# Optimization experiments

Measured on AMD Instinct MI355X. Metric: run time of the kernel, lower is better.

Reference implementation:

```python
import jax, jax.numpy as jnp
import numpy as np

B, S, H, D = 2, 2048, 16, 128
HID = H * D
ROPE_BASE = 10000.0


def _rope_tables(seq_len, dim, dtype):
    inv_freq = 1.0 / (ROPE_BASE ** (jnp.arange(0, dim, 2, dtype=jnp.float32) / dim))
    t = jnp.arange(seq_len, dtype=jnp.float32)
    freqs = jnp.einsum('s,d->sd', t, inv_freq)          # [S, D/2]
    emb = jnp.concatenate([freqs, freqs], axis=-1)       # [S, D]
    return jnp.cos(emb).astype(dtype), jnp.sin(emb).astype(dtype)


def _rotate_half(x):
    x1, x2 = jnp.split(x, 2, axis=-1)
    return jnp.concatenate([-x2, x1], axis=-1)


def _apply_rope(x, cos, sin, position_ids):
    # x: [B,H,S,D]; cos/sin: [S_emb, D]; position_ids: [B,S] or [1,S]
    c = cos[position_ids][:, None, :, :]  # [B,1,S,D]
    s = sin[position_ids][:, None, :, :]
    return x * c + _rotate_half(x) * s


def setup_inputs() -> dict:
    key = jax.random.key(0)
    ks = jax.random.split(key, 9)
    hidden_states = jax.random.normal(ks[0], (B, S, HID), jnp.float32) * 0.02
    Wq = jax.random.normal(ks[1], (HID, HID), jnp.float32) * 0.02
    Wk = jax.random.normal(ks[2], (HID, HID), jnp.float32) * 0.02
    Wv = jax.random.normal(ks[3], (HID, HID), jnp.float32) * 0.02
    Wo = jax.random.normal(ks[4], (HID, HID), jnp.float32) * 0.02
    # binary mask marking summary tokens
    sum_mask = jax.random.randint(ks[5], (B, S), 0, 2).astype(jnp.float32)
    # row-stochastic-ish averaging matrix over tokens (KV compression weights)
    raw = jax.random.uniform(ks[6], (B, S, S), jnp.float32)
    sum_attn_mask = sum_mask[:, :, None] * raw / jnp.sum(raw, axis=-1, keepdims=True)
    # additive causal mask [B,1,S,S]
    causal = jnp.tril(jnp.ones((S, S), dtype=bool))
    attention_mask = jnp.where(causal, 0.0, -1e9).astype(jnp.float32)
    attention_mask = jnp.broadcast_to(attention_mask[None, None], (B, 1, S, S))
    position_ids = jnp.broadcast_to(jnp.arange(S, dtype=jnp.int32), (B, S))
    return {
        'hidden_states': hidden_states, 'sum_mask': sum_mask,
        'sum_attn_mask': sum_attn_mask, 'attention_mask': attention_mask,
        'position_ids': position_ids, 'Wq': Wq, 'Wk': Wk, 'Wv': Wv, 'Wo': Wo,
    }


def reference(hidden_states, sum_mask, sum_attn_mask, attention_mask,
              position_ids, Wq, Wk, Wv, Wo):
    dtype = hidden_states.dtype
    # projections (F.linear: x @ W^T), then [B,H,S,D]
    def proj(W):
        return (hidden_states @ W.T).reshape(B, S, H, D).transpose(0, 2, 1, 3)
    q, k, v = proj(Wq), proj(Wk), proj(Wv)

    kv_seq_len = S
    cos, sin = _rope_tables(kv_seq_len, D, dtype)
    q = _apply_rope(q, cos, sin, position_ids)

    # KV compression: weighted token averaging injected at summary positions
    k_avg = jnp.einsum('bqk,bhkd->bhqd', sum_attn_mask, k)
    v_avg = jnp.einsum('bqk,bhkd->bhqd', sum_attn_mask, v)
    no_sum = (1.0 - sum_mask)[:, None, :, None]  # [B,1,S,1]
    k = no_sum * k + k_avg
    v = no_sum * v + v_avg

    key_pos = jnp.arange(kv_seq_len, dtype=jnp.int32)[None, :]  # [1,S]
    k = _apply_rope(k, cos, sin, key_pos)

    scale = 1.0 / np.sqrt(D)
    attn = jnp.einsum('bhqd,bhkd->bhqk', q, k) * scale
    attn = attn + attention_mask
    attn = jnp.maximum(attn, jnp.finfo(attn.dtype).min)
    attn = jax.nn.softmax(attn.astype(jnp.float32), axis=-1).astype(dtype)
    out = jnp.einsum('bhqk,bhkd->bhqd', attn, v)            # [B,H,S,D]
    out = out.transpose(0, 2, 1, 3).reshape(B, S, HID)
    return out @ Wo.T
```

## Files before the change

### kernel.cpp

```cpp
#include <hip/hip_runtime.h>
#include <cstdint>
#include <cstddef>

#define B_   2
#define S_   2048
#define H_   16
#define D_   128
#define HID_ 2048

typedef __bf16 bf16;
typedef unsigned short u16;
typedef bf16 bf16x4 __attribute__((ext_vector_type(4)));
typedef bf16 bf16x8 __attribute__((ext_vector_type(8)));
typedef u16  u16x8  __attribute__((ext_vector_type(8)));
typedef float f32x4 __attribute__((ext_vector_type(4)));

__device__ unsigned g_work;

__device__ __forceinline__ f32x4 mfma16(bf16x8 a, bf16x8 b, f32x4 c){
  return __builtin_amdgcn_mfma_f32_16x16x32_bf16(a, b, c, 0, 0, 0);
}

__device__ __forceinline__ void gload_lds16(const void* g, void* l){
  __builtin_amdgcn_global_load_lds((const __attribute__((address_space(1))) void*)g,
                                   (__attribute__((address_space(3))) void*)l, 16, 0, 0);
}

__device__ __forceinline__ void bar_lgkm(){
  asm volatile("s_waitcnt lgkmcnt(0)" ::: "memory");
  __builtin_amdgcn_s_barrier();
}
__device__ __forceinline__ void bar_full(){
  asm volatile("s_waitcnt vmcnt(0) lgkmcnt(0)" ::: "memory");
  __builtin_amdgcn_s_barrier();
}

__global__ void k_tables(float* __restrict__ cosT, float* __restrict__ sinT){
  if (blockIdx.x == 0 && threadIdx.x == 0) g_work = 0u;
  int id = blockIdx.x*256 + threadIdx.x;
  int p = id >> 6, i = id & 63;
  double f = (double)p * pow(10000.0, -(double)i/64.0);
  cosT[id] = (float)cos(f);
  sinT[id] = (float)sin(f);
}

__global__ void k_cvt_all(const float* __restrict__ a0, bf16* __restrict__ o0,
                          const float* __restrict__ a1, bf16* __restrict__ o1,
                          const float* __restrict__ w0, bf16* __restrict__ q0,
                          const float* __restrict__ w1, bf16* __restrict__ q1,
                          const float* __restrict__ w2, bf16* __restrict__ q2,
                          const float* __restrict__ w3, bf16* __restrict__ q3){
  const float* src; bf16* dst; int n4;
  switch (blockIdx.y){
    case 0: src = a0; dst = o0; n4 = 2097152; break;
    case 1: src = a1; dst = o1; n4 = 2097152; break;
    case 2: src = w0; dst = q0; n4 = 1048576; break;
    case 3: src = w1; dst = q1; n4 = 1048576; break;
    case 4: src = w2; dst = q2; n4 = 1048576; break;
    default: src = w3; dst = q3; n4 = 1048576; break;
  }
  int i = blockIdx.x*256 + threadIdx.x;
  if (i >= n4) return;
  f32x4 v = *reinterpret_cast<const f32x4*>(src + (size_t)i*4);
  bf16x4 o;
  o[0]=(bf16)v[0]; o[1]=(bf16)v[1]; o[2]=(bf16)v[2]; o[3]=(bf16)v[3];
  *reinterpret_cast<bf16x4*>(dst + (size_t)i*4) = o;
}

__global__ __launch_bounds__(256) void k_transpose_cvt(const float* __restrict__ in, bf16* __restrict__ out){
  __shared__ bf16 t[64][72];
  const int tid = threadIdx.x;
  const int b = blockIdx.z, j0 = blockIdx.x*64, s0 = blockIdx.y*64;
  #pragma unroll
  for (int u0 = 0; u0 < 4; ++u0){
    int u = u0*256 + tid;
    int r = u >> 4, c4 = (u & 15)*4;
    f32x4 v = *reinterpret_cast<const f32x4*>(in + ((size_t)b*S_ + s0 + r)*HID_ + j0 + c4);
    bf16x4 o; o[0]=(bf16)v[0]; o[1]=(bf16)v[1]; o[2]=(bf16)v[2]; o[3]=(bf16)v[3];
    *reinterpret_cast<bf16x4*>(&t[r][c4]) = o;
  }
  __syncthreads();
  #pragma unroll
  for (int u0 = 0; u0 < 4; ++u0){
    int u = u0*256 + tid;
    int r = u >> 4, c4 = (u & 15)*4;
    bf16x4 o;
    o[0] = t[c4+0][r]; o[1] = t[c4+1][r]; o[2] = t[c4+2][r]; o[3] = t[c4+3][r];
    *reinterpret_cast<bf16x4*>(out + ((size_t)b*HID_ + j0 + r)*S_ + s0 + c4) = o;
  }
}

template<int EPI>
__global__ __launch_bounds__(256) void k_gemm_nt(
    const bf16* __restrict__ A, const bf16* __restrict__ Bm, void* __restrict__ Cv,
    int Kd, size_t sAz, size_t sBz, size_t sCz, int N,
    const float* __restrict__ mask, const float* __restrict__ hid)
{
  const int tid = threadIdx.x;
  const int wid = tid >> 6, lane = tid & 63;
  const int g = lane >> 4, li = lane & 15;
  const int z = blockIdx.z;
  const int m0 = blockIdx.y*128, n0 = blockIdx.x*128;
  const int wm = wid >> 1, wn = wid & 1;
  const bf16* Ab = A + (size_t)z*sAz;
  const bf16* Bb = Bm + (size_t)z*sBz;

  __shared__ bf16 lA[128*64];
  __shared__ bf16 lB[128*64];

  f32x4 acc[4][4];
  #pragma unroll
  for (int i=0;i<4;++i)
    #pragma unroll
    for (int j=0;j<4;++j)
      acc[i][j] = {0.f,0.f,0.f,0.f};

  for (int k0 = 0; k0 < Kd; k0 += 64){
    #pragma unroll
    for (int j=0;j<4;++j){
      int ci = j*256 + tid;
      int r = ci >> 3, cb = ci & 7;
      gload_lds16(Ab + (size_t)(m0 + r)*Kd + k0 + cb*8, (char*)lA + (j*256 + wid*64)*16);
      gload_lds16(Bb + (size_t)(n0 + r)*Kd + k0 + cb*8, (char*)lB + (j*256 + wid*64)*16);
    }
    __syncthreads();
    #pragma unroll
    for (int kk=0;kk<2;++kk){
      bf16x8 af[4], bfm[4];
      #pragma unroll
      for (int i=0;i<4;++i){
        af[i]  = *reinterpret_cast<const bf16x8*>(&lA[(wm*64 + i*16 + li)*64 + kk*32 + g*8]);
        bfm[i] = *reinterpret_cast<const bf16x8*>(&lB[(wn*64 + i*16 + li)*64 + kk*32 + g*8]);
      }
      #pragma unroll
      for (int i=0;i<4;++i)
        #pragma unroll
        for (int j=0;j<4;++j)
          acc[i][j] = mfma16(af[i], bfm[j], acc[i][j]);
    }
    __syncthreads();
  }

  #pragma unroll
  for (int i=0;i<4;++i){
    #pragma unroll
    for (int j=0;j<4;++j){
      #pragma unroll
      for (int v=0;v<4;++v){
        int row = m0 + wm*64 + i*16 + g*4 + v;
        int col = n0 + wn*64 + j*16 + li;
        float x = acc[i][j][v];
        if (EPI == 1){
          x += (1.f - mask[z*S_ + row]) * hid[((size_t)z*S_ + row)*HID_ + col];
          ((bf16*)Cv)[(size_t)z*sCz + (size_t)row*N + col] = (bf16)x;
        } else if (EPI == 0){
          ((bf16*)Cv)[(size_t)row*N + col] = (bf16)x;
        } else if (EPI == 2){
          ((float*)Cv)[(size_t)row*N + col] = x;
        } else {
          if (n0 < 2048) ((bf16*)Cv)[(size_t)row*2048 + col] = (bf16)x;
          else ((bf16*)(void*)hid)[(size_t)row*2048 + col - 2048] = (bf16)x;
        }
      }
    }
  }
}

template<int EPI>
__global__ __launch_bounds__(512,2) void k_gemm256(
    const bf16* __restrict__ A, const bf16* __restrict__ Bm, void* __restrict__ Cv,
    int Kd, size_t sAz, size_t sBz, size_t sCz, int N,
    const float* __restrict__ mask, const float* __restrict__ hid)
{
  const int tid = threadIdx.x;
  const int wid = tid >> 6, lane = tid & 63;
  const int g = lane >> 4, li = lane & 15;
  const int wm = wid >> 2, wn = wid & 3;
  const int z = blockIdx.z;
  const int m0 = blockIdx.y*256, n0 = blockIdx.x*256;
  const bf16* Ab = A + (size_t)z*sAz + (size_t)m0*Kd;
  const bf16* Bb = Bm + (size_t)z*sBz + (size_t)n0*Kd;

  __shared__ bf16 lA[2][256*64];
  __shared__ bf16 lB[2][256*64];

  const int rr0 = tid >> 3, cc = tid & 7;
  const int rr1 = rr0 + 64;
  const int cx0 = cc ^ (rr0 & 7);
  const int cx1 = cc ^ (rr1 & 7);

  f32x4 acc[8][4];
  #pragma unroll
  for (int i=0;i<8;++i)
    #pragma unroll
    for (int j=0;j<4;++j) acc[i][j] = {0.f,0.f,0.f,0.f};

  auto stage = [&](int buf, int kt, int matsel, int half){
    const bf16* s = matsel ? Bb : Ab;
    char* dbase = (char*)(matsel ? lB[buf] : lA[buf]) + half*16384;
    gload_lds16(s + (size_t)(half*128 + rr0)*Kd + kt*64 + cx0*8, dbase + (wid*64)*16);
    gload_lds16(s + (size_t)(half*128 + rr1)*Kd + kt*64 + cx1*8, dbase + (512 + wid*64)*16);
  };
  auto rdA = [&](int buf, int i, int kh){
    int row = wm*128 + i*16 + li;
    return *reinterpret_cast<const bf16x8*>((const char*)lA[buf] + row*128 + (((kh*4 + g) ^ (row & 7))*16));
  };
  auto rdB = [&](int buf, int j, int kh){
    int row = wn*64 + j*16 + li;
    return *reinterpret_cast<const bf16x8*>((const char*)lB[buf] + row*128 + (((kh*4 + g) ^ (row & 7))*16));
  };

  const int NT = Kd >> 6;
  stage(0,0,0,0); stage(0,0,0,1); stage(0,0,1,0); stage(0,0,1,1);
  __syncthreads();

  int cur = 0;
  for (int kt = 0; kt < NT; ++kt){
    const bool more = (kt+1 < NT);
    bf16x8 af[4], bfr[4];

    if (more){
      stage(cur^1, kt+1, 0, 0); stage(cur^1, kt+1, 0, 1);
      stage(cur^1, kt+1, 1, 0); stage(cur^1, kt+1, 1, 1);
    }
    #pragma unroll
    for (int i=0;i<4;++i) af[i] = rdA(cur, i, 0);
    #pragma unroll
    for (int j=0;j<4;++j) bfr[j] = rdB(cur, j, 0);
    __builtin_amdgcn_s_setprio(1);
    #pragma unroll
    for (int i=0;i<4;++i)
      #pragma unroll
      for (int j=0;j<4;++j) acc[i][j] = mfma16(af[i], bfr[j], acc[i][j]);
    __builtin_amdgcn_s_setprio(0);
    __builtin_amdgcn_s_barrier();

    #pragma unroll
    for (int i=0;i<4;++i) af[i] = rdA(cur, i+4, 0);
    __builtin_amdgcn_s_setprio(1);
    #pragma unroll
    for (int i=0;i<4;++i)
      #pragma unroll
      for (int j=0;j<4;++j) acc[i+4][j] = mfma16(af[i], bfr[j], acc[i+4][j]);
    __builtin_amdgcn_s_setprio(0);
    __builtin_amdgcn_s_barrier();

    #pragma unroll
    for (int i=0;i<4;++i) af[i] = rdA(cur, i, 1);
    #pragma unroll
    for (int j=0;j<4;++j) bfr[j] = rdB(cur, j, 1);
    __builtin_amdgcn_s_setprio(1);
    #pragma unroll
    for (int i=0;i<4;++i)
      #pragma unroll
      for (int j=0;j<4;++j) acc[i][j] = mfma16(af[i], bfr[j], acc[i][j]);
    __builtin_amdgcn_s_setprio(0);
    __builtin_amdgcn_s_barrier();

    #pragma unroll
    for (int i=0;i<4;++i) af[i] = rdA(cur, i+4, 1);
    __builtin_amdgcn_s_setprio(1);
    #pragma unroll
    for (int i=0;i<4;++i)
      #pragma unroll
      for (int j=0;j<4;++j) acc[i+4][j] = mfma16(af[i], bfr[j], acc[i+4][j]);
    __builtin_amdgcn_s_setprio(0);

    __syncthreads();
    cur ^= 1;
  }

  #pragma unroll
  for (int i=0;i<8;++i){
    #pragma unroll
    for (int j=0;j<4;++j){
      #pragma unroll
      for (int v=0;v<4;++v){
        int row = m0 + wm*128 + i*16 + g*4 + v;
        int col = n0 + wn*64 + j*16 + li;
        float x = acc[i][j][v];
        if (EPI == 1){
          x += (1.f - mask[z*S_ + row]) * hid[((size_t)z*S_ + row)*HID_ + col];
          ((bf16*)Cv)[(size_t)z*sCz + (size_t)row*N + col] = (bf16)x;
        } else if (EPI == 0){
          ((bf16*)Cv)[(size_t)row*N + col] = (bf16)x;
        } else if (EPI == 2){
          ((float*)Cv)[(size_t)row*N + col] = x;
        } else {
          if (n0 < 2048) ((bf16*)Cv)[(size_t)row*2048 + col] = (bf16)x;
          else ((bf16*)(void*)hid)[(size_t)row*2048 + col - 2048] = (bf16)x;
        }
      }
    }
  }
}

__global__ void k_rope(bf16* __restrict__ X, const float* __restrict__ cosT,
                       const float* __restrict__ sinT, const int* __restrict__ pos){
  int id = blockIdx.x*256 + threadIdx.x;
  int d4 = (id & 15)*4;
  int h  = (id >> 4) & 15;
  int s  = (id >> 8) & 2047;
  int b  = id >> 19;
  int p = pos ? pos[b*S_ + s] : s;
  size_t base = (((size_t)b*S_ + s)*H_ + h)*D_ + d4;
  f32x4 c  = *reinterpret_cast<const f32x4*>(cosT + (size_t)p*64 + d4);
  f32x4 sn = *reinterpret_cast<const f32x4*>(sinT + (size_t)p*64 + d4);
  bf16x4 x1 = *reinterpret_cast<bf16x4*>(X + base);
  bf16x4 x2 = *reinterpret_cast<bf16x4*>(X + base + 64);
  bf16x4 o1, o2;
  #pragma unroll
  for (int i=0;i<4;++i){
    float a = (float)x1[i], bb = (float)x2[i];
    o1[i] = (bf16)(a*c[i] - bb*sn[i]);
    o2[i] = (bf16)(bb*c[i] + a*sn[i]);
  }
  *reinterpret_cast<bf16x4*>(X + base) = o1;
  *reinterpret_cast<bf16x4*>(X + base + 64) = o2;
}

__global__ __launch_bounds__(512,2) void k_flash(const bf16* __restrict__ Q, const bf16* __restrict__ K,
                                                 const bf16* __restrict__ V, bf16* __restrict__ O,
                                                 bf16* __restrict__ OPb, float* __restrict__ ML)
{
  const int tid = threadIdx.x;
  const int wid = tid >> 6, lane = tid & 63;
  const int g = lane >> 4, li = lane & 15;

  __shared__ bf16 Klds[2][64*128];
  __shared__ char VtB[128*128];
  __shared__ bf16 Plds[8][32*72];
  __shared__ int s_item;

  const int dc = tid & 15, kvp = tid >> 4;

  for (;;) {
    if (tid == 0) s_item = (int)atomicAdd(&g_work, 1u);
    __syncthreads();
    const int w = s_item;
    if (w >= 384) return;

    int qx, bh, part, t0, t1;
    if (w < 64)       { qx = 7; int u = w;       bh = u>>1; part = u&1; t0 = part?16:0; t1 = part?32:16; }
    else if (w < 96)  { qx = 3; bh = w-64;  part = -1; t0 = 0; t1 = 16; }
    else if (w < 160) { qx = 6; int u = w-96;  bh = u>>1; part = u&1; t0 = part?14:0; t1 = part?28:14; }
    else if (w < 224) { qx = 5; int u = w-160; bh = u>>1; part = u&1; t0 = part?12:0; t1 = part?24:12; }
    else if (w < 256) { qx = 2; bh = w-224; part = -1; t0 = 0; t1 = 12; }
    else if (w < 320) { qx = 4; int u = w-256; bh = u>>1; part = u&1; t0 = part?10:0; t1 = part?20:10; }
    else if (w < 352) { qx = 1; bh = w-320; part = -1; t0 = 0; t1 = 8; }
    else              { qx = 0; bh = w-352; part = -1; t0 = 0; t1 = 4; }

    const int qb = qx * 256;
    const size_t headoff = ((size_t)(bh >> 4)*S_*H_ + (bh & 15))*D_;
    const bf16* Kh = K + headoff;
    const u16*  Vh = (const u16*)(V + headoff);

    bf16x8 qf[2][4];
    #pragma unroll
    for (int rb=0;rb<2;++rb){
      const bf16* Qp = Q + headoff + (size_t)(qb + wid*32 + rb*16 + li)*H_*D_;
      #pragma unroll
      for (int kc=0;kc<4;++kc)
        qf[rb][kc] = *reinterpret_cast<const bf16x8*>(Qp + kc*32 + g*8);
    }

    float mrun[2][4], lrun[2][4];
    f32x4 acc[2][8];
    #pragma unroll
    for (int rb=0;rb<2;++rb){
      #pragma unroll
      for (int v=0;v<4;++v){ mrun[rb][v] = -1e30f; lrun[rb][v] = 0.f; }
      #pragma unroll
      for (int fn=0;fn<8;++fn) acc[rb][fn] = {0.f,0.f,0.f,0.f};
    }

    u16x8 vp[2];
    auto stageK = [&](int buf, int t){
      #pragma unroll
      for (int j=0;j<2;++j){
        int ci = j*512 + tid;
        int r = ci >> 4, cb = ci & 15;
        const char* src = (const char*)(Kh + (size_t)(t*64 + r)*H_*D_) + ((cb ^ (r & 7)) * 16);
        gload_lds16(src, (char*)Klds[buf] + (j*512 + wid*64)*16);
      }
    };
    auto loadV = [&](int t){
      const u16* sp = Vh + (size_t)(t*64 + kvp*2)*H_*D_ + dc*8;
      vp[0] = *reinterpret_cast<const u16x8*>(sp);
      vp[1] = *reinterpret_cast<const u16x8*>(sp + H_*D_);
    };
    auto writeVtB = [&](){
      #pragma unroll
      for (int e=0;e<8;++e){
        int r = dc*8 + e;
        int swz = (r ^ (r >> 3)) & 7;
        int addr = r*128 + (((kvp >> 2) ^ swz) << 4) + ((kvp << 2) & 12);
        *reinterpret_cast<uint32_t*>(VtB + addr) =
            (uint32_t)vp[0][e] | ((uint32_t)vp[1][e] << 16);
      }
    };

    stageK(0, t0);
    loadV(t0);
    writeVtB();
    bar_full();

    int cur = 0;
    for (int t=t0; t<t1; ++t){
      const bool more = (t+1 < t1);
      if (more){ stageK(cur^1, t+1); loadV(t+1); }

      f32x4 sc[2][4];
      #pragma unroll
      for (int fc=0;fc<4;++fc){
        int r = fc*16 + li;
        bf16x8 kf[4];
        #pragma unroll
        for (int kc=0;kc<4;++kc)
          kf[kc] = *reinterpret_cast<const bf16x8*>((const char*)Klds[cur] + r*256 + (((4*kc + g) ^ (r & 7))*16));
        __builtin_amdgcn_s_setprio(1);
        #pragma unroll
        for (int rb=0;rb<2;++rb){
          f32x4 s = {0.f,0.f,0.f,0.f};
          #pragma unroll
          for (int kc=0;kc<4;++kc)
            s = mfma16(qf[rb][kc], kf[kc], s);
          sc[rb][fc] = s;
        }
        __builtin_amdgcn_s_setprio(0);
      }

      const float scale = 0.08838834764831845f;
      const int c0 = t*64;
      if (t >= 4*qx){
        #pragma unroll
        for (int rb=0;rb<2;++rb){
          const int rowg = qb + wid*32 + rb*16 + g*4;
          #pragma unroll
          for (int fc=0;fc<4;++fc){
            int col = c0 + fc*16 + li;
            #pragma unroll
            for (int v=0;v<4;++v){
              float s = sc[rb][fc][v] * scale;
              sc[rb][fc][v] = (col > rowg + v) ? -1e30f : s;
            }
          }
        }
      } else {
        #pragma unroll
        for (int rb=0;rb<2;++rb)
          #pragma unroll
          for (int fc=0;fc<4;++fc)
            #pragma unroll
            for (int v=0;v<4;++v)
              sc[rb][fc][v] *= scale;
      }

      #pragma unroll
      for (int rb=0;rb<2;++rb){
        float tm[4];
        #pragma unroll
        for (int v=0;v<4;++v){
          float m2 = fmaxf(fmaxf(sc[rb][0][v], sc[rb][1][v]), fmaxf(sc[rb][2][v], sc[rb][3][v]));
          m2 = fmaxf(m2, __shfl_xor(m2, 1));
          m2 = fmaxf(m2, __shfl_xor(m2, 2));
          m2 = fmaxf(m2, __shfl_xor(m2, 4));
          m2 = fmaxf(m2, __shfl_xor(m2, 8));
          tm[v] = m2;
        }
        bool need = false;
        #pragma unroll
        for (int v=0;v<4;++v) need = need || (tm[v] > mrun[rb][v] + 8.f);
        if (__any(need)){
          float al[4];
          #pragma unroll
          for (int v=0;v<4;++v){
            float mnew = fmaxf(mrun[rb][v], tm[v]);
            al[v] = __expf(mrun[rb][v] - mnew);
            mrun[rb][v] = mnew;
            lrun[rb][v] *= al[v];
          }
          #pragma unroll
          for (int fn=0;fn<8;++fn)
            #pragma unroll
            for (int v=0;v<4;++v) acc[rb][fn][v] *= al[v];
        }
        float rs[4] = {0.f,0.f,0.f,0.f};
        #pragma unroll
        for (int fc=0;fc<4;++fc){
          #pragma unroll
          for (int v=0;v<4;++v){
            float p = __expf(sc[rb][fc][v] - mrun[rb][v]);
            rs[v] += p;
            Plds[wid][(rb*16 + g*4 + v)*72 + fc*16 + li] = (bf16)p;
          }
        }
        #pragma unroll
        for (int v=0;v<4;++v){
          float r = rs[v];
          r += __shfl_xor(r, 1); r += __shfl_xor(r, 2);
          r += __shfl_xor(r, 4); r += __shfl_xor(r, 8);
          lrun[rb][v] += r;
        }
      }

      bf16x8 pa[2][2];
      #pragma unroll
      for (int rb=0;rb<2;++rb)
        #pragma unroll
        for (int kc=0;kc<2;++kc)
          pa[rb][kc] = *reinterpret_cast<const bf16x8*>(&Plds[wid][(rb*16 + li)*72 + kc*32 + g*8]);
      #pragma unroll
      for (int fn=0;fn<8;++fn){
        int r = fn*16 + li;
        int swz = (r ^ (r >> 3)) & 7;
        bf16x8 bv[2];
        #pragma unroll
        for (int kc=0;kc<2;++kc)
          bv[kc] = *reinterpret_cast<const bf16x8*>(VtB + r*128 + (((kc*4 + g) ^ swz) << 4));
        __builtin_amdgcn_s_setprio(1);
        #pragma unroll
        for (int rb=0;rb<2;++rb)
          #pragma unroll
          for (int kc=0;kc<2;++kc)
            acc[rb][fn] = mfma16(pa[rb][kc], bv[kc], acc[rb][fn]);
        __builtin_amdgcn_s_setprio(0);
      }

      if (more){
        bar_lgkm();
        writeVtB();
      }
      bar_full();
      cur ^= 1;
    }

    if (part < 0){
      #pragma unroll
      for (int rb=0;rb<2;++rb){
        #pragma unroll
        for (int v=0;v<4;++v){
          float inv = 1.f / lrun[rb][v];
          int row = qb + wid*32 + rb*16 + g*4 + v;
          bf16* dst = O + headoff + (size_t)row*H_*D_ + li;
          #pragma unroll
          for (int fn=0;fn<8;++fn)
            dst[fn*16] = (bf16)(acc[rb][fn][v] * inv);
        }
      }
    } else {
      const int sidx = ((qx-4)<<6) + (bh<<1) + part;
      bf16* Od = OPb + (size_t)sidx*256*128;
      float* MLd = ML + (size_t)sidx*512;
      #pragma unroll
      for (int rb=0;rb<2;++rb){
        #pragma unroll
        for (int v=0;v<4;++v){
          float inv = 1.f / lrun[rb][v];
          int rl = wid*32 + rb*16 + g*4 + v;
          #pragma unroll
          for (int fn=0;fn<8;++fn)
            Od[rl*128 + fn*16 + li] = (bf16)(acc[rb][fn][v] * inv);
          if (li == 0){
            MLd[rl*2 + 0] = mrun[rb][v];
            MLd[rl*2 + 1] = lrun[rb][v];
          }
        }
      }
    }
  }
}

__global__ __launch_bounds__(256) void k_merge(const bf16* __restrict__ OPb, const float* __restrict__ ML,
                                               bf16* __restrict__ O){
  const int gid = blockIdx.x;
  const int qx = 4 + (gid >> 5);
  const int bh = gid & 31;
  const int s0 = ((qx-4)<<6) + (bh<<1), s1 = s0 + 1;
  const int b = bh >> 4, h = bh & 15;
  const int qb = qx * 256;
  const int row = threadIdx.x;

  float m0 = ML[(size_t)s0*512 + row*2], l0 = ML[(size_t)s0*512 + row*2 + 1];
  float m1 = ML[(size_t)s1*512 + row*2], l1 = ML[(size_t)s1*512 + row*2 + 1];
  float mm = fmaxf(m0, m1);
  float w0 = l0 * __expf(m0 - mm), w1 = l1 * __expf(m1 - mm);
  float inv = 1.f / (w0 + w1);
  w0 *= inv; w1 *= inv;
  const bf16* r0 = OPb + ((size_t)s0*256 + row)*128;
  const bf16* r1 = OPb + ((size_t)s1*256 + row)*128;
  bf16* dst = O + (((size_t)b*S_ + qb + row)*H_ + h)*D_;
  #pragma unroll
  for (int c=0; c<128; c+=8){
    bf16x8 a = *reinterpret_cast<const bf16x8*>(r0 + c);
    bf16x8 bq = *reinterpret_cast<const bf16x8*>(r1 + c);
    bf16x8 o;
    #pragma unroll
    for (int i=0;i<8;++i) o[i] = (bf16)((float)a[i]*w0 + (float)bq[i]*w1);
    *reinterpret_cast<bf16x8*>(dst + c) = o;
  }
}

extern "C" void kernel_launch(void* const* d_in, const int* in_sizes, int n_in,
                              void* d_out, int out_size, void* d_ws, size_t ws_size,
                              hipStream_t stream)
{
  (void)in_sizes; (void)n_in; (void)out_size; (void)ws_size;
  const float* hid   = (const float*)d_in[0];
  const float* smask = (const float*)d_in[1];
  const float* samat = (const float*)d_in[2];
  const int*   pos   = (const int*)d_in[4];
  const float* Wq = (const float*)d_in[5];
  const float* Wk = (const float*)d_in[6];
  const float* Wv = (const float*)d_in[7];
  const float* Wo = (const float*)d_in[8];
  float* out = (float*)d_out;
  char* ws = (char*)d_ws;

  const size_t SZ_TAB = (size_t)S_*64*4;
  const size_t SZ_BSH = (size_t)B_*S_*HID_*2;
  float* cosT = (float*)(ws);
  float* sinT = (float*)(ws + SZ_TAB);
  bf16* buf1 = (bf16*)(ws + 2*SZ_TAB);
  bf16* buf2 = (bf16*)(ws + 2*SZ_TAB + 1*SZ_BSH);
  bf16* buf3 = (bf16*)(ws + 2*SZ_TAB + 2*SZ_BSH);
  bf16* buf4 = (bf16*)(ws + 2*SZ_TAB + 3*SZ_BSH);
  bf16* Wqb = (bf16*)(ws + 2*SZ_TAB + 4*SZ_BSH);
  bf16* Wkb = Wqb + (size_t)HID_*HID_;
  bf16* Wvb = Wkb + (size_t)HID_*HID_;
  bf16* Wob = Wvb + (size_t)HID_*HID_;
  bf16* OPb = Wqb;
  float* ML = (float*)(Wqb + (size_t)256*256*128);

  k_tables<<<512,256,0,stream>>>(cosT, sinT);
  k_cvt_all<<<dim3(8192,6),256,0,stream>>>(hid, buf1, samat, buf3,
                                           Wq, Wqb, Wk, Wkb, Wv, Wvb, Wo, Wob);
  k_transpose_cvt<<<dim3(32,32,2),256,0,stream>>>(hid, buf2);

  const size_t sBat = (size_t)S_*HID_;
  k_gemm_nt<1><<<dim3(16,16,2),256,0,stream>>>(buf3, buf2, buf4, 2048, sBat, sBat, sBat, 2048, smask, hid);
  k_gemm_nt<0><<<dim3(16,32,1),256,0,stream>>>(buf1, Wqb, buf3, 2048, 0,0,0, 2048, nullptr, nullptr);
  k_rope<<<4096,256,0,stream>>>(buf3, cosT, sinT, pos);
  k_gemm256<3><<<dim3(16,16,1),512,0,stream>>>(buf4, Wkb, buf2, 2048, 0,0,0, 2048, nullptr, (const float*)buf1);
  k_rope<<<4096,256,0,stream>>>(buf2, cosT, sinT, nullptr);
  k_flash<<<dim3(256),512,0,stream>>>(buf3, buf2, buf1, buf4, OPb, ML);
  k_merge<<<dim3(128),256,0,stream>>>(OPb, ML, buf4);
  k_gemm_nt<2><<<dim3(16,32,1),256,0,stream>>>(buf4, Wob, out, 2048, 0,0,0, 2048, nullptr, nullptr);
}
```

Baseline: 413.8 us.

## Split flash attention into finer table-driven work items with multi-way merge

```diff
diff --git a/kernel.cpp b/kernel.cpp
--- a/kernel.cpp
+++ b/kernel.cpp
@@ -16,6 +16,15 @@
 typedef float f32x4 __attribute__((ext_vector_type(4)));
 
 __device__ unsigned g_work;
+
+__device__ const int it_qx[18]  = {4,4,6,6,6,7,7,7,7,5,5,5,3,3,1,2,2,0};
+__device__ const int it_t0[18]  = {0,10,0,10,19,0,8,16,24,0,8,16,0,8,0,0,6,0};
+__device__ const int it_t1[18]  = {10,20,10,19,28,8,16,24,32,8,16,24,8,16,8,6,12,4};
+__device__ const int it_dst[18] = {0,1,0,2,3,0,4,5,6,0,7,8,0,9,0,0,10,0};
+__device__ const int mg_qx[6]  = {4,6,7,5,3,2};
+__device__ const int mg_np[6]  = {2,3,4,3,2,2};
+__device__ const int mg_ml0[6] = {0,2,5,9,12,15};
+__device__ const int mg_ss[6]  = {0,1,3,6,8,9};
 
 __device__ __forceinline__ f32x4 mfma16(bf16x8 a, bf16x8 b, f32x4 c){
   return __builtin_amdgcn_mfma_f32_16x16x32_bf16(a, b, c, 0, 0, 0);
@@ -296,7 +305,7 @@
 }
 
 __global__ void k_rope(bf16* __restrict__ X, const float* __restrict__ cosT,
-                       const float* __restrict__ sinT, const int* __restrict__ pos){
+                       const float* __restrict__ sinT, const int* __restrict__ pos, float scale){
   int id = blockIdx.x*256 + threadIdx.x;
   int d4 = (id & 15)*4;
   int h  = (id >> 4) & 15;
@@ -312,14 +321,14 @@
   #pragma unroll
   for (int i=0;i<4;++i){
     float a = (float)x1[i], bb = (float)x2[i];
-    o1[i] = (bf16)(a*c[i] - bb*sn[i]);
-    o2[i] = (bf16)(bb*c[i] + a*sn[i]);
+    o1[i] = (bf16)((a*c[i] - bb*sn[i])*scale);
+    o2[i] = (bf16)((bb*c[i] + a*sn[i])*scale);
   }
   *reinterpret_cast<bf16x4*>(X + base) = o1;
   *reinterpret_cast<bf16x4*>(X + base + 64) = o2;
 }
 
-__global__ __launch_bounds__(512,2) void k_flash(const bf16* __restrict__ Q, const bf16* __restrict__ K,
+__global__ __launch_bounds__(512,4) void k_flash(const bf16* __restrict__ Q, const bf16* __restrict__ K,
                                                  const bf16* __restrict__ V, bf16* __restrict__ O,
                                                  bf16* __restrict__ OPb, float* __restrict__ ML)
 {
@@ -329,26 +338,19 @@
 
   __shared__ bf16 Klds[2][64*128];
   __shared__ char VtB[128*128];
-  __shared__ bf16 Plds[8][32*72];
-  __shared__ int s_item;
+  __shared__ bf16 Plds[8][32*64];
+  int* sip = (int*)&Plds[0][0];
 
   const int dc = tid & 15, kvp = tid >> 4;
 
   for (;;) {
-    if (tid == 0) s_item = (int)atomicAdd(&g_work, 1u);
+    if (tid == 0) *sip = (int)atomicAdd(&g_work, 1u);
     __syncthreads();
-    const int w = s_item;
-    if (w >= 384) return;
-
-    int qx, bh, part, t0, t1;
-    if (w < 64)       { qx = 7; int u = w;       bh = u>>1; part = u&1; t0 = part?16:0; t1 = part?32:16; }
-    else if (w < 96)  { qx = 3; bh = w-64;  part = -1; t0 = 0; t1 = 16; }
-    else if (w < 160) { qx = 6; int u = w-96;  bh = u>>1; part = u&1; t0 = part?14:0; t1 = part?28:14; }
-    else if (w < 224) { qx = 5; int u = w-160; bh = u>>1; part = u&1; t0 = part?12:0; t1 = part?24:12; }
-    else if (w < 256) { qx = 2; bh = w-224; part = -1; t0 = 0; t1 = 12; }
-    else if (w < 320) { qx = 4; int u = w-256; bh = u>>1; part = u&1; t0 = part?10:0; t1 = part?20:10; }
-    else if (w < 352) { qx = 1; bh = w-320; part = -1; t0 = 0; t1 = 8; }
-    else              { qx = 0; bh = w-352; part = -1; t0 = 0; t1 = 4; }
+    const int w = *sip;
+    if (w >= 576) return;
+
+    const int idx = w >> 5, bh = w & 31;
+    const int qx = it_qx[idx], t0 = it_t0[idx], t1 = it_t1[idx];
 
     const int qb = qx * 256;
     const size_t headoff = ((size_t)(bh >> 4)*S_*H_ + (bh & 15))*D_;
@@ -430,7 +432,6 @@
         __builtin_amdgcn_s_setprio(0);
       }
 
-      const float scale = 0.08838834764831845f;
       const int c0 = t*64;
       if (t >= 4*qx){
         #pragma unroll
@@ -440,20 +441,10 @@
           for (int fc=0;fc<4;++fc){
             int col = c0 + fc*16 + li;
             #pragma unroll
-            for (int v=0;v<4;++v){
-              float s = sc[rb][fc][v] * scale;
-              sc[rb][fc][v] = (col > rowg + v) ? -1e30f : s;
-            }
+            for (int v=0;v<4;++v)
+              if (col > rowg + v) sc[rb][fc][v] = -1e30f;
           }
         }
-      } else {
-        #pragma unroll
-        for (int rb=0;rb<2;++rb)
-          #pragma unroll
-          for (int fc=0;fc<4;++fc)
-            #pragma unroll
-            for (int v=0;v<4;++v)
-              sc[rb][fc][v] *= scale;
       }
 
       #pragma unroll
@@ -492,7 +483,9 @@
           for (int v=0;v<4;++v){
             float p = __expf(sc[rb][fc][v] - mrun[rb][v]);
             rs[v] += p;
-            Plds[wid][(rb*16 + g*4 + v)*72 + fc*16 + li] = (bf16)p;
+            int prow = rb*16 + g*4 + v;
+            int pchunk = (fc*2 + (li>>3)) ^ (prow & 7);
+            Plds[wid][prow*64 + pchunk*8 + (li & 7)] = (bf16)p;
           }
         }
         #pragma unroll
@@ -509,7 +502,8 @@
       for (int rb=0;rb<2;++rb)
         #pragma unroll
         for (int kc=0;kc<2;++kc)
-          pa[rb][kc] = *reinterpret_cast<const bf16x8*>(&Plds[wid][(rb*16 + li)*72 + kc*32 + g*8]);
+          pa[rb][kc] = *reinterpret_cast<const bf16x8*>(
+              &Plds[wid][(rb*16 + li)*64 + (((kc*4 + g) ^ (li & 7))<<3)]);
       #pragma unroll
       for (int fn=0;fn<8;++fn){
         int r = fn*16 + li;
@@ -535,36 +529,34 @@
       cur ^= 1;
     }
 
-    if (part < 0){
-      #pragma unroll
-      for (int rb=0;rb<2;++rb){
-        #pragma unroll
-        for (int v=0;v<4;++v){
-          float inv = 1.f / lrun[rb][v];
-          int row = qb + wid*32 + rb*16 + g*4 + v;
-          bf16* dst = O + headoff + (size_t)row*H_*D_ + li;
-          #pragma unroll
-          for (int fn=0;fn<8;++fn)
-            dst[fn*16] = (bf16)(acc[rb][fn][v] * inv);
-        }
-      }
-    } else {
-      const int sidx = ((qx-4)<<6) + (bh<<1) + part;
-      bf16* Od = OPb + (size_t)sidx*256*128;
-      float* MLd = ML + (size_t)sidx*512;
+    const int dsel = it_dst[idx];
+    float* MLd = ML + (size_t)(bh*18 + idx)*512;
+    if (dsel == 0){
       #pragma unroll
       for (int rb=0;rb<2;++rb){
         #pragma unroll
         for (int v=0;v<4;++v){
           float inv = 1.f / lrun[rb][v];
           int rl = wid*32 + rb*16 + g*4 + v;
+          bf16* dst = O + headoff + (size_t)(qb + rl)*H_*D_ + li;
+          #pragma unroll
+          for (int fn=0;fn<8;++fn)
+            dst[fn*16] = (bf16)(acc[rb][fn][v] * inv);
+          if (li == 0){ MLd[rl*2] = mrun[rb][v]; MLd[rl*2+1] = lrun[rb][v]; }
+        }
+      }
+    } else {
+      bf16* Od = OPb + (size_t)(bh*10 + dsel - 1)*256*128;
+      #pragma unroll
+      for (int rb=0;rb<2;++rb){
+        #pragma unroll
+        for (int v=0;v<4;++v){
+          float inv = 1.f / lrun[rb][v];
+          int rl = wid*32 + rb*16 + g*4 + v;
           #pragma unroll
           for (int fn=0;fn<8;++fn)
             Od[rl*128 + fn*16 + li] = (bf16)(acc[rb][fn][v] * inv);
-          if (li == 0){
-            MLd[rl*2 + 0] = mrun[rb][v];
-            MLd[rl*2 + 1] = lrun[rb][v];
-          }
+          if (li == 0){ MLd[rl*2] = mrun[rb][v]; MLd[rl*2+1] = lrun[rb][v]; }
         }
       }
     }
@@ -574,29 +566,53 @@
 __global__ __launch_bounds__(256) void k_merge(const bf16* __restrict__ OPb, const float* __restrict__ ML,
                                                bf16* __restrict__ O){
   const int gid = blockIdx.x;
-  const int qx = 4 + (gid >> 5);
-  const int bh = gid & 31;
-  const int s0 = ((qx-4)<<6) + (bh<<1), s1 = s0 + 1;
+  const int gsel = gid >> 5, bh = gid & 31;
+  const int qx = mg_qx[gsel], np = mg_np[gsel], ml0 = mg_ml0[gsel], ss = mg_ss[gsel];
   const int b = bh >> 4, h = bh & 15;
-  const int qb = qx * 256;
   const int row = threadIdx.x;
 
-  float m0 = ML[(size_t)s0*512 + row*2], l0 = ML[(size_t)s0*512 + row*2 + 1];
-  float m1 = ML[(size_t)s1*512 + row*2], l1 = ML[(size_t)s1*512 + row*2 + 1];
-  float mm = fmaxf(m0, m1);
-  float w0 = l0 * __expf(m0 - mm), w1 = l1 * __expf(m1 - mm);
-  float inv = 1.f / (w0 + w1);
-  w0 *= inv; w1 *= inv;
-  const bf16* r0 = OPb + ((size_t)s0*256 + row)*128;
-  const bf16* r1 = OPb + ((size_t)s1*256 + row)*128;
-  bf16* dst = O + (((size_t)b*S_ + qb + row)*H_ + h)*D_;
-  #pragma unroll
-  for (int c=0; c<128; c+=8){
-    bf16x8 a = *reinterpret_cast<const bf16x8*>(r0 + c);
-    bf16x8 bq = *reinterpret_cast<const bf16x8*>(r1 + c);
+  float m[4], l[4], wgt[4];
+  #pragma unroll
+  for (int j=0;j<4;++j){
+    if (j < np){
+      const float* mlp = ML + (size_t)(bh*18 + ml0 + j)*512 + row*2;
+      m[j] = mlp[0]; l[j] = mlp[1];
+    } else { m[j] = -1e30f; l[j] = 0.f; }
+  }
+  float mm = fmaxf(fmaxf(m[0], m[1]), fmaxf(m[2], m[3]));
+  float wsum = 0.f;
+  #pragma unroll
+  for (int j=0;j<4;++j){ wgt[j] = l[j]*__expf(m[j]-mm); wsum += wgt[j]; }
+  float inv = 1.f/wsum;
+  #pragma unroll
+  for (int j=0;j<4;++j) wgt[j] *= inv;
+
+  bf16* dst = O + (((size_t)b*S_ + qx*256 + row)*H_ + h)*D_;
+  const bf16* s1 = OPb + (size_t)(bh*10 + ss + 0)*256*128 + row*128;
+  const bf16* s2 = OPb + (size_t)(bh*10 + ss + 1)*256*128 + row*128;
+  const bf16* s3 = OPb + (size_t)(bh*10 + ss + 2)*256*128 + row*128;
+  #pragma unroll
+  for (int c=0;c<128;c+=8){
+    bf16x8 a = *reinterpret_cast<const bf16x8*>(dst + c);
+    float acc8[8];
+    #pragma unroll
+    for (int i=0;i<8;++i) acc8[i] = (float)a[i]*wgt[0];
+    bf16x8 p1 = *reinterpret_cast<const bf16x8*>(s1 + c);
+    #pragma unroll
+    for (int i=0;i<8;++i) acc8[i] += (float)p1[i]*wgt[1];
+    if (np > 2){
+      bf16x8 p2 = *reinterpret_cast<const bf16x8*>(s2 + c);
+      #pragma unroll
+      for (int i=0;i<8;++i) acc8[i] += (float)p2[i]*wgt[2];
+    }
+    if (np > 3){
+      bf16x8 p3 = *reinterpret_cast<const bf16x8*>(s3 + c);
+      #pragma unroll
+      for (int i=0;i<8;++i) acc8[i] += (float)p3[i]*wgt[3];
+    }
     bf16x8 o;
     #pragma unroll
-    for (int i=0;i<8;++i) o[i] = (bf16)((float)a[i]*w0 + (float)bq[i]*w1);
+    for (int i=0;i<8;++i) o[i] = (bf16)acc8[i];
     *reinterpret_cast<bf16x8*>(dst + c) = o;
   }
 }
@@ -630,7 +646,7 @@
   bf16* Wvb = Wkb + (size_t)HID_*HID_;
   bf16* Wob = Wvb + (size_t)HID_*HID_;
   bf16* OPb = Wqb;
-  float* ML = (float*)(Wqb + (size_t)256*256*128);
+  float* ML = (float*)((char*)Wqb + (size_t)320*256*128*2);
 
   k_tables<<<512,256,0,stream>>>(cosT, sinT);
   k_cvt_all<<<dim3(8192,6),256,0,stream>>>(hid, buf1, samat, buf3,
@@ -640,10 +656,10 @@
   const size_t sBat = (size_t)S_*HID_;
   k_gemm_nt<1><<<dim3(16,16,2),256,0,stream>>>(buf3, buf2, buf4, 2048, sBat, sBat, sBat, 2048, smask, hid);
   k_gemm_nt<0><<<dim3(16,32,1),256,0,stream>>>(buf1, Wqb, buf3, 2048, 0,0,0, 2048, nullptr, nullptr);
-  k_rope<<<4096,256,0,stream>>>(buf3, cosT, sinT, pos);
+  k_rope<<<4096,256,0,stream>>>(buf3, cosT, sinT, pos, 0.08838834764831845f);
   k_gemm256<3><<<dim3(16,16,1),512,0,stream>>>(buf4, Wkb, buf2, 2048, 0,0,0, 2048, nullptr, (const float*)buf1);
-  k_rope<<<4096,256,0,stream>>>(buf2, cosT, sinT, nullptr);
-  k_flash<<<dim3(256),512,0,stream>>>(buf3, buf2, buf1, buf4, OPb, ML);
-  k_merge<<<dim3(128),256,0,stream>>>(OPb, ML, buf4);
+  k_rope<<<4096,256,0,stream>>>(buf2, cosT, sinT, nullptr, 1.0f);
+  k_flash<<<dim3(512),512,0,stream>>>(buf3, buf2, buf1, buf4, OPb, ML);
+  k_merge<<<dim3(192),256,0,stream>>>(OPb, ML, buf4);
   k_gemm_nt<2><<<dim3(16,32,1),256,0,stream>>>(buf4, Wob, out, 2048, 0,0,0, 2048, nullptr, nullptr);
 }
```

Result: slower. 806.6 us (+94.9%).
